# Kernel optimization log

Measured on AMD Instinct MI355X. Metric: run time of the kernel, lower is better.

Reference implementation:

```python
import jax, jax.numpy as jnp
import numpy as np

K = 20  # max_similar_relations


def setup_inputs() -> dict:
    key = jax.random.key(0)
    k1, k2 = jax.random.split(key)
    B, R, D = 256, 2048, 64
    x = jax.random.normal(k1, (B, R, D), dtype=jnp.float32)
    query_rels = jax.random.randint(k2, (B,), 0, R, dtype=jnp.int32)
    return {
        "x": x,
        "query_rels": query_rels,
        # raw params as in __init__: threshold_init=0.2 -> raw=0.2*2-1=-0.6; strength_init=0.05 -> raw=0.05*5-1=-0.75
        "threshold_raw": jnp.float32(-0.6),
        "strength_raw": jnp.float32(-0.75),
        "weight_scale": jnp.float32(1.0),
        "temperature": jnp.float32(1.0),
    }


def reference(x, query_rels, threshold_raw, strength_raw, weight_scale, temperature):
    B, R, D = x.shape
    bidx = jnp.arange(B)
    threshold = jax.nn.sigmoid(threshold_raw)
    strength = jax.nn.sigmoid(strength_raw) * 0.2
    temp = jnp.clip(temperature, 0.1, 10.0)

    # F.normalize(x, p=2, dim=2)
    norms = x / jnp.maximum(jnp.linalg.norm(x, axis=2, keepdims=True), 1e-12)

    q = norms[bidx, query_rels]                      # [B, D] normalized query reprs
    sims = jnp.einsum("bd,brd->br", q, norms)        # [B, R] cosine similarities
    sims = sims.at[bidx, query_rels].set(-1.0)       # exclude self
    sim_w = jax.nn.sigmoid((sims - threshold) * 10.0)

    topv, topi = jax.lax.top_k(sims, K)              # [B, K]
    valid = (topv > threshold) & (topi != query_rels[:, None])

    # softmax over valid top-k entries only (per batch row)
    logits = jnp.where(valid, topv / temp, -1e9)
    w = jax.nn.softmax(logits, axis=1)
    w = jnp.where(valid, w, 0.0)

    sw = jnp.take_along_axis(sim_w, topi, axis=1)    # smooth sigmoid weights of selected
    combined = w * sw
    adjusted = combined * (1.0 + weight_scale * topv)
    adjusted = adjusted / (jnp.sum(adjusted, axis=1, keepdims=True) + 1e-8)

    # gather top-k normalized reprs and weighted-sum them
    top_reprs = jnp.take_along_axis(norms, jnp.broadcast_to(topi[:, :, None], (B, K, D)), axis=1)
    weighted = jnp.einsum("bk,bkd->bd", adjusted, top_reprs)  # [B, D]

    q_orig = x[bidx, query_rels]                     # original (unnormalized) query repr
    has_valid = jnp.any(valid, axis=1, keepdims=True)
    mixed = (1.0 - strength) * q_orig + strength * weighted
    new_q = jnp.where(has_valid, mixed, q_orig)

    return x.at[bidx, query_rels].set(new_q)
```

## Files before the change

kernel.cpp:

```cpp
#include <hip/hip_runtime.h>
#include <math.h>

#define KTOP 20

__global__ void qnorm_kernel(const float* __restrict__ x,
                             const int* __restrict__ qrels,
                             float* __restrict__ qn, int R) {
    int b = blockIdx.x;
    int t = threadIdx.x;
    int qr = qrels[b];
    float v = x[((long)b * R + qr) * 64 + t];
    float ss = v * v;
#pragma unroll
    for (int m = 1; m < 64; m <<= 1) ss += __shfl_xor(ss, m, 64);
    float dn = fmaxf(sqrtf(ss), 1e-12f);
    qn[b * 64 + t] = v / dn;
}

__global__ void copy_sims_kernel(const float* __restrict__ x,
                                 const int* __restrict__ qrels,
                                 const float* __restrict__ qn,
                                 float* __restrict__ out,
                                 float* __restrict__ sims,
                                 float* __restrict__ dnorm, int R) {
    int b = blockIdx.y;
    int t = threadIdx.x;
    int row = blockIdx.x * 16 + (t >> 4);
    int l16 = t & 15;
    if (row >= R) return;

    long base = ((long)b * R + row) * 64 + l16 * 4;
    const float4 v = *(const float4*)(x + base);
    *(float4*)(out + base) = v;

    const float4 q = *(const float4*)(qn + b * 64 + l16 * 4);
    float dot = v.x * q.x + v.y * q.y + v.z * q.z + v.w * q.w;
    float ss  = v.x * v.x + v.y * v.y + v.z * v.z + v.w * v.w;
#pragma unroll
    for (int m = 1; m < 16; m <<= 1) {
        dot += __shfl_xor(dot, m, 64);
        ss  += __shfl_xor(ss,  m, 64);
    }
    if (l16 == 0) {
        float dn = fmaxf(sqrtf(ss), 1e-12f);
        int qr = qrels[b];
        sims[(long)b * R + row]  = (row == qr) ? -1.0f : dot / dn;
        dnorm[(long)b * R + row] = dn;
    }
}

__global__ void finalize_kernel(const float* __restrict__ x,
                                const int* __restrict__ qrels,
                                const float* __restrict__ sims,
                                const float* __restrict__ dnorm,
                                const float* __restrict__ thr_raw,
                                const float* __restrict__ str_raw,
                                const float* __restrict__ wscale_p,
                                const float* __restrict__ temp_p,
                                float* __restrict__ out, int R) {
    extern __shared__ float smem[];
    float* s_val  = smem;
    float* red_v  = s_val + R;
    int*   red_i  = (int*)(red_v + 256);
    float* s_topv = (float*)(red_i + 256);
    int*   s_topi = (int*)(s_topv + KTOP);
    float* s_adj  = (float*)(s_topi + KTOP);
    float* s_misc = s_adj + KTOP;

    int b = blockIdx.x;
    int t = threadIdx.x;

    for (int i = t; i < R; i += 256) s_val[i] = sims[(long)b * R + i];
    __syncthreads();

    for (int k = 0; k < KTOP; ++k) {
        float bv = -INFINITY;
        int   bi = R;
        for (int i = t; i < R; i += 256) {
            float v = s_val[i];
            if (v > bv) { bv = v; bi = i; }
        }
        red_v[t] = bv; red_i[t] = bi;
        __syncthreads();
        for (int s = 128; s > 0; s >>= 1) {
            if (t < s) {
                float v2 = red_v[t + s]; int i2 = red_i[t + s];
                if (v2 > red_v[t] || (v2 == red_v[t] && i2 < red_i[t])) {
                    red_v[t] = v2; red_i[t] = i2;
                }
            }
            __syncthreads();
        }
        if (t == 0) {
            s_topv[k] = red_v[0];
            s_topi[k] = red_i[0];
            s_val[red_i[0]] = -INFINITY;
        }
        __syncthreads();
    }

    if (t == 0) {
        float threshold = 1.0f / (1.0f + expf(-thr_raw[0]));
        float strength  = (1.0f / (1.0f + expf(-str_raw[0]))) * 0.2f;
        float temp = fminf(fmaxf(temp_p[0], 0.1f), 10.0f);
        float wsc  = wscale_p[0];
        int   qr   = qrels[b];

        float tv[KTOP]; int ti[KTOP]; bool valid[KTOP];
        bool has_valid = false;
        float m = -INFINITY;
        for (int k = 0; k < KTOP; ++k) {
            tv[k] = s_topv[k]; ti[k] = s_topi[k];
            valid[k] = (tv[k] > threshold) && (ti[k] != qr);
            if (valid[k]) { has_valid = true; m = fmaxf(m, tv[k] / temp); }
        }
        if (has_valid) {
            float w[KTOP], wsum = 0.0f;
            for (int k = 0; k < KTOP; ++k) {
                w[k] = valid[k] ? expf(tv[k] / temp - m) : 0.0f;
                wsum += w[k];
            }
            float adj[KTOP], asum = 0.0f;
            for (int k = 0; k < KTOP; ++k) {
                float wk = w[k] / wsum;
                float sw = 1.0f / (1.0f + expf(-(tv[k] - threshold) * 10.0f));
                float a  = wk * sw * (1.0f + wsc * tv[k]);
                adj[k] = a; asum += a;
            }
            for (int k = 0; k < KTOP; ++k) {
                float dn = dnorm[(long)b * R + ti[k]];
                s_adj[k] = (adj[k] / (asum + 1e-8f)) / dn;
            }
        } else {
            for (int k = 0; k < KTOP; ++k) s_adj[k] = 0.0f;
        }
        s_misc[0] = strength;
        s_misc[1] = has_valid ? 1.0f : 0.0f;
    }
    __syncthreads();

    if (t < 64) {
        int qr = qrels[b];
        long qb = ((long)b * R + qr) * 64 + t;
        float qo = x[qb];
        float res = qo;
        if (s_misc[1] > 0.5f) {
            float acc = 0.0f;
#pragma unroll
            for (int k = 0; k < KTOP; ++k)
                acc += s_adj[k] * x[((long)b * R + s_topi[k]) * 64 + t];
            float st = s_misc[0];
            res = (1.0f - st) * qo + st * acc;
        }
        out[qb] = res;
    }
}

extern "C" void kernel_launch(void* const* d_in, const int* in_sizes, int n_in,
                              void* d_out, int out_size, void* d_ws, size_t ws_size,
                              hipStream_t stream) {
    const float* x      = (const float*)d_in[0];
    const int*   qrels  = (const int*)d_in[1];
    const float* thr    = (const float*)d_in[2];
    const float* str    = (const float*)d_in[3];
    const float* wscale = (const float*)d_in[4];
    const float* temp   = (const float*)d_in[5];
    float* out = (float*)d_out;

    const int B = in_sizes[1];
    const int D = 64;
    const int R = in_sizes[0] / (B * D);

    float* qn    = (float*)d_ws;
    float* sims  = qn + (size_t)B * 64;
    float* dnorm = sims + (size_t)B * R;

    qnorm_kernel<<<B, 64, 0, stream>>>(x, qrels, qn, R);

    dim3 grid2((R + 15) / 16, B);
    copy_sims_kernel<<<grid2, 256, 0, stream>>>(x, qrels, qn, out, sims, dnorm, R);

    size_t shmem = (size_t)(R + 512 + 3 * KTOP + 2) * 4 + 64;
    finalize_kernel<<<B, 256, shmem, stream>>>(x, qrels, sims, dnorm,
                                               thr, str, wscale, temp, out, R);
}
```

Measured before the change: 276.1 us.

## Fuse enhancer into single kernel with threshold-filtered top-k candidates

Replaces the three kernels (query normalise, copy plus similarities, top-k finalize) with one block-per-batch kernel. Similarities and norms are kept in shared memory instead of global workspace, and only rows above the threshold are collected as candidates through a shared atomic counter. A wave-level top-k runs only when there are more candidates than K; otherwise the candidates are used as-is. This removes the 20 rounds of block-wide reductions and synchronisations over all R rows, but it limits the copy phase to 256 blocks of 1024 threads and assumes R is at most 2048.

```diff
diff --git a/kernel.cpp b/kernel.cpp
--- a/kernel.cpp
+++ b/kernel.cpp
@@ -2,157 +2,138 @@
 #include <math.h>
 
 #define KTOP 20
+#define R_MAX 2048
 
-__global__ void qnorm_kernel(const float* __restrict__ x,
-                             const int* __restrict__ qrels,
-                             float* __restrict__ qn, int R) {
-    int b = blockIdx.x;
-    int t = threadIdx.x;
-    int qr = qrels[b];
-    float v = x[((long)b * R + qr) * 64 + t];
-    float ss = v * v;
+__global__ __launch_bounds__(1024) void fused_enhancer(
+    const float* __restrict__ x,
+    const int* __restrict__ qrels,
+    const float* __restrict__ thr_raw,
+    const float* __restrict__ str_raw,
+    const float* __restrict__ wscale_p,
+    const float* __restrict__ temp_p,
+    float* __restrict__ out, int R)
+{
+    __shared__ float s_q[64];
+    __shared__ float s_sims[R_MAX];
+    __shared__ float s_dn[R_MAX];
+    __shared__ int   s_cand[R_MAX];
+    __shared__ int   s_ncand;
+    __shared__ float s_topv[KTOP];
+    __shared__ int   s_topi[KTOP];
+    __shared__ float s_adj[KTOP];
+    __shared__ float s_strength;
+
+    const int b = blockIdx.x;
+    const int t = threadIdx.x;
+    const int qr = qrels[b];
+    const float threshold = 1.0f / (1.0f + expf(-thr_raw[0]));
+
+    if (t == 0) s_ncand = 0;
+
+    if (t < 64) {
+        float v = x[((long)b * R + qr) * 64 + t];
+        float ss = v * v;
 #pragma unroll
-    for (int m = 1; m < 64; m <<= 1) ss += __shfl_xor(ss, m, 64);
-    float dn = fmaxf(sqrtf(ss), 1e-12f);
-    qn[b * 64 + t] = v / dn;
-}
-
-__global__ void copy_sims_kernel(const float* __restrict__ x,
-                                 const int* __restrict__ qrels,
-                                 const float* __restrict__ qn,
-                                 float* __restrict__ out,
-                                 float* __restrict__ sims,
-                                 float* __restrict__ dnorm, int R) {
-    int b = blockIdx.y;
-    int t = threadIdx.x;
-    int row = blockIdx.x * 16 + (t >> 4);
-    int l16 = t & 15;
-    if (row >= R) return;
-
-    long base = ((long)b * R + row) * 64 + l16 * 4;
-    const float4 v = *(const float4*)(x + base);
-    *(float4*)(out + base) = v;
-
-    const float4 q = *(const float4*)(qn + b * 64 + l16 * 4);
-    float dot = v.x * q.x + v.y * q.y + v.z * q.z + v.w * q.w;
-    float ss  = v.x * v.x + v.y * v.y + v.z * v.z + v.w * v.w;
-#pragma unroll
-    for (int m = 1; m < 16; m <<= 1) {
-        dot += __shfl_xor(dot, m, 64);
-        ss  += __shfl_xor(ss,  m, 64);
+        for (int m = 1; m < 64; m <<= 1) ss += __shfl_xor(ss, m, 64);
+        s_q[t] = v / fmaxf(sqrtf(ss), 1e-12f);
     }
-    if (l16 == 0) {
-        float dn = fmaxf(sqrtf(ss), 1e-12f);
-        int qr = qrels[b];
-        sims[(long)b * R + row]  = (row == qr) ? -1.0f : dot / dn;
-        dnorm[(long)b * R + row] = dn;
-    }
-}
-
-__global__ void finalize_kernel(const float* __restrict__ x,
-                                const int* __restrict__ qrels,
-                                const float* __restrict__ sims,
-                                const float* __restrict__ dnorm,
-                                const float* __restrict__ thr_raw,
-                                const float* __restrict__ str_raw,
-                                const float* __restrict__ wscale_p,
-                                const float* __restrict__ temp_p,
-                                float* __restrict__ out, int R) {
-    extern __shared__ float smem[];
-    float* s_val  = smem;
-    float* red_v  = s_val + R;
-    int*   red_i  = (int*)(red_v + 256);
-    float* s_topv = (float*)(red_i + 256);
-    int*   s_topi = (int*)(s_topv + KTOP);
-    float* s_adj  = (float*)(s_topi + KTOP);
-    float* s_misc = s_adj + KTOP;
-
-    int b = blockIdx.x;
-    int t = threadIdx.x;
-
-    for (int i = t; i < R; i += 256) s_val[i] = sims[(long)b * R + i];
     __syncthreads();
 
-    for (int k = 0; k < KTOP; ++k) {
-        float bv = -INFINITY;
-        int   bi = R;
-        for (int i = t; i < R; i += 256) {
-            float v = s_val[i];
-            if (v > bv) { bv = v; bi = i; }
+    const int grp = t >> 4, l16 = t & 15;
+    const float4 q4 = *(const float4*)(s_q + l16 * 4);
+    const long xbase = (long)b * R * 64;
+    for (int row = grp; row < R; row += 64) {
+        long base = xbase + (long)row * 64 + l16 * 4;
+        const float4 v = *(const float4*)(x + base);
+        *(float4*)(out + base) = v;
+        float dot = v.x * q4.x + v.y * q4.y + v.z * q4.z + v.w * q4.w;
+        float ss  = v.x * v.x + v.y * v.y + v.z * v.z + v.w * v.w;
+#pragma unroll
+        for (int m = 1; m < 16; m <<= 1) {
+            dot += __shfl_xor(dot, m, 64);
+            ss  += __shfl_xor(ss,  m, 64);
         }
-        red_v[t] = bv; red_i[t] = bi;
-        __syncthreads();
-        for (int s = 128; s > 0; s >>= 1) {
-            if (t < s) {
-                float v2 = red_v[t + s]; int i2 = red_i[t + s];
-                if (v2 > red_v[t] || (v2 == red_v[t] && i2 < red_i[t])) {
-                    red_v[t] = v2; red_i[t] = i2;
+        if (l16 == 0) {
+            float dn  = fmaxf(sqrtf(ss), 1e-12f);
+            float sim = (row == qr) ? -1.0f : dot / dn;
+            s_sims[row] = sim;
+            s_dn[row]   = dn;
+            if (sim > threshold) {
+                int p = atomicAdd(&s_ncand, 1);
+                s_cand[p] = row;
+            }
+        }
+    }
+    __syncthreads();
+
+    const int ncand = s_ncand;
+    const int ksel = ncand < KTOP ? ncand : KTOP;
+
+    if (t < 64) {
+        if (ncand > KTOP) {
+            float lv[32]; int li[32];
+#pragma unroll
+            for (int j = 0; j < 32; ++j) {
+                int i = t + 64 * j;
+                if (i < ncand) { li[j] = s_cand[i]; lv[j] = s_sims[li[j]]; }
+                else           { li[j] = 0x7fffffff; lv[j] = -INFINITY; }
+            }
+            for (int k = 0; k < KTOP; ++k) {
+                float bv = -INFINITY; int bi = 0x7fffffff;
+#pragma unroll
+                for (int j = 0; j < 32; ++j) {
+                    if (lv[j] > bv || (lv[j] == bv && li[j] < bi)) { bv = lv[j]; bi = li[j]; }
                 }
+#pragma unroll
+                for (int m = 1; m < 64; m <<= 1) {
+                    float v2 = __shfl_xor(bv, m, 64);
+                    int   i2 = __shfl_xor(bi, m, 64);
+                    if (v2 > bv || (v2 == bv && i2 < bi)) { bv = v2; bi = i2; }
+                }
+#pragma unroll
+                for (int j = 0; j < 32; ++j) if (li[j] == bi) lv[j] = -INFINITY;
+                if (t == 0) { s_topv[k] = bv; s_topi[k] = bi; }
             }
-            __syncthreads();
+        } else if (t == 0) {
+            for (int k = 0; k < ksel; ++k) {
+                int idx = s_cand[k];
+                s_topi[k] = idx;
+                s_topv[k] = s_sims[idx];
+            }
         }
-        if (t == 0) {
-            s_topv[k] = red_v[0];
-            s_topi[k] = red_i[0];
-            s_val[red_i[0]] = -INFINITY;
-        }
-        __syncthreads();
     }
 
     if (t == 0) {
-        float threshold = 1.0f / (1.0f + expf(-thr_raw[0]));
-        float strength  = (1.0f / (1.0f + expf(-str_raw[0]))) * 0.2f;
+        float strength = (1.0f / (1.0f + expf(-str_raw[0]))) * 0.2f;
         float temp = fminf(fmaxf(temp_p[0], 0.1f), 10.0f);
         float wsc  = wscale_p[0];
-        int   qr   = qrels[b];
-
-        float tv[KTOP]; int ti[KTOP]; bool valid[KTOP];
-        bool has_valid = false;
-        float m = -INFINITY;
-        for (int k = 0; k < KTOP; ++k) {
-            tv[k] = s_topv[k]; ti[k] = s_topi[k];
-            valid[k] = (tv[k] > threshold) && (ti[k] != qr);
-            if (valid[k]) { has_valid = true; m = fmaxf(m, tv[k] / temp); }
-        }
-        if (has_valid) {
-            float w[KTOP], wsum = 0.0f;
-            for (int k = 0; k < KTOP; ++k) {
-                w[k] = valid[k] ? expf(tv[k] / temp - m) : 0.0f;
-                wsum += w[k];
-            }
-            float adj[KTOP], asum = 0.0f;
-            for (int k = 0; k < KTOP; ++k) {
-                float wk = w[k] / wsum;
-                float sw = 1.0f / (1.0f + expf(-(tv[k] - threshold) * 10.0f));
-                float a  = wk * sw * (1.0f + wsc * tv[k]);
+        if (ksel > 0) {
+            float m = -INFINITY;
+            for (int k = 0; k < ksel; ++k) m = fmaxf(m, s_topv[k] / temp);
+            float w[KTOP]; float wsum = 0.0f;
+            for (int k = 0; k < ksel; ++k) { w[k] = expf(s_topv[k] / temp - m); wsum += w[k]; }
+            float adj[KTOP]; float asum = 0.0f;
+            for (int k = 0; k < ksel; ++k) {
+                float tv = s_topv[k];
+                float sw = 1.0f / (1.0f + expf(-(tv - threshold) * 10.0f));
+                float a  = (w[k] / wsum) * sw * (1.0f + wsc * tv);
                 adj[k] = a; asum += a;
             }
-            for (int k = 0; k < KTOP; ++k) {
-                float dn = dnorm[(long)b * R + ti[k]];
-                s_adj[k] = (adj[k] / (asum + 1e-8f)) / dn;
-            }
-        } else {
-            for (int k = 0; k < KTOP; ++k) s_adj[k] = 0.0f;
+            for (int k = 0; k < ksel; ++k)
+                s_adj[k] = (adj[k] / (asum + 1e-8f)) / s_dn[s_topi[k]];
         }
-        s_misc[0] = strength;
-        s_misc[1] = has_valid ? 1.0f : 0.0f;
+        s_strength = strength;
     }
     __syncthreads();
 
-    if (t < 64) {
-        int qr = qrels[b];
+    if (t < 64 && ksel > 0) {
         long qb = ((long)b * R + qr) * 64 + t;
         float qo = x[qb];
-        float res = qo;
-        if (s_misc[1] > 0.5f) {
-            float acc = 0.0f;
-#pragma unroll
-            for (int k = 0; k < KTOP; ++k)
-                acc += s_adj[k] * x[((long)b * R + s_topi[k]) * 64 + t];
-            float st = s_misc[0];
-            res = (1.0f - st) * qo + st * acc;
-        }
-        out[qb] = res;
+        float acc = 0.0f;
+        for (int k = 0; k < ksel; ++k)
+            acc += s_adj[k] * x[((long)b * R + s_topi[k]) * 64 + t];
+        float st = s_strength;
+        out[qb] = (1.0f - st) * qo + st * acc;
     }
 }
 
@@ -170,17 +151,7 @@
     const int B = in_sizes[1];
     const int D = 64;
     const int R = in_sizes[0] / (B * D);
+    (void)D; (void)d_ws; (void)ws_size;
 
-    float* qn    = (float*)d_ws;
-    float* sims  = qn + (size_t)B * 64;
-    float* dnorm = sims + (size_t)B * R;
-
-    qnorm_kernel<<<B, 64, 0, stream>>>(x, qrels, qn, R);
-
-    dim3 grid2((R + 15) / 16, B);
-    copy_sims_kernel<<<grid2, 256, 0, stream>>>(x, qrels, qn, out, sims, dnorm, R);
-
-    size_t shmem = (size_t)(R + 512 + 3 * KTOP + 2) * 4 + 64;
-    finalize_kernel<<<B, 256, shmem, stream>>>(x, qrels, sims, dnorm,
-                                               thr, str, wscale, temp, out, R);
+    fused_enhancer<<<B, 1024, 0, stream>>>(x, qrels, thr, str, wscale, temp, out, R);
 }
```

After: 253.0 us. 8.4% less time.
